# Performance work log

Measured on AMD Instinct MI355X. Metric: run time of the kernel, lower is better.

Reference implementation:

```python
import jax, jax.numpy as jnp
import numpy as np

N, IN, HID, OUT, HD = 512, 256, 256, 256, 64  # n_agents, in_dim, hid_dim, out_dim, head_dim (out_dim // n_heads)


def _mlp2(x, w1, b1, w2, b2):
    return jax.nn.relu(x @ w1.T + b1) @ w2.T + b2


def setup_inputs():
    key = jax.random.key(0)
    ks = jax.random.split(key, 32)
    p = lambda i, shape: jax.random.normal(ks[i], shape, dtype=jnp.float32) * 0.05
    V = jax.random.normal(ks[0], (N, IN), dtype=jnp.float32)
    adj = jax.random.randint(ks[1], (N, N), 0, 2, dtype=jnp.int32)
    adj = adj.at[jnp.arange(N), jnp.arange(N)].set(1)  # self-loops so no softmax row is all -inf
    prev_hidden = jax.random.normal(ks[2], (N, HID), dtype=jnp.float32)
    return {
        "V": V, "adj": adj, "prev_hidden": prev_hidden,
        "W1": p(3, (HID, IN)), "sa0": p(4, (HID,)), "sa1": p(5, (HID,)),
        "ce_w1": p(6, (HID, 2 * IN)), "ce_b1": p(7, (HID,)), "ce_w2": p(8, (HD, HID)), "ce_b2": p(9, (HD,)),
        "ca0": p(10, (HD,)), "ca1": p(11, (HD,)),
        "te_w1": p(12, (HID, IN + HID)), "te_b1": p(13, (HID,)), "te_w2": p(14, (HD, HID)), "te_b2": p(15, (HD,)),
        "ta0": p(16, (HD,)), "ta1": p(17, (HD,)),
        "pe_w1": p(18, (HID, 3 * IN)), "pe_b1": p(19, (HID,)), "pe_w2": p(20, (HD, HID)), "pe_b2": p(21, (HD,)),
        "pa0": p(22, (HD,)), "pa1": p(23, (HD,)),
        "W2": p(24, (OUT, HID + 2 * HD + 1)), "op_w": p(25, (OUT, OUT)), "op_b": p(26, (OUT,)),
        "ln_g": jnp.ones((OUT,), jnp.float32), "ln_b": jnp.zeros((OUT,), jnp.float32),
    }


def _forward(V, adj, prev_hidden, W1, sa0, sa1, ce_w1, ce_b1, ce_w2, ce_b2, ca0, ca1,
             te_w1, te_b1, te_w2, te_b2, ta0, ta1, pe_w1, pe_b1, pe_w2, pe_b2, pa0, pa1,
             W2, op_w, op_b, ln_g, ln_b):
    neg = -jnp.inf
    # --- branch 1: standard GAT attention ---
    Wh1 = V @ W1.T                                             # (N, HID)
    s1 = (Wh1 @ sa0)[:, None] + (Wh1 @ sa1)[None, :]           # (N, N)
    s1 = jnp.where(adj == 0, neg, s1)
    H1 = jax.nn.softmax(s1, axis=1) @ Wh1                      # (N, HID)
    # --- branch 2: causal, all ordered pairs i != j ---
    wA, wB = ce_w1[:, :IN], ce_w1[:, IN:]
    h = jax.nn.relu((V @ wA.T)[:, None, :] + (V @ wB.T)[None, :, :] + ce_b1)  # (N, N, HID)
    f = h @ ce_w2.T + ce_b2                                    # (N, N, HD)
    s2 = jnp.where(jnp.eye(N, dtype=bool), neg, f @ (ca0 + ca1))
    a2 = jax.nn.softmax(s2.reshape(-1)).reshape(N, N)          # softmax over all off-diagonal pairs
    H2 = jnp.broadcast_to(jnp.einsum('ij,ijd->d', a2, f), (N, HD))
    # --- branch 3: temporal; (N,1) scores broadcast against (N,N) causal mask ---
    tf = _mlp2(jnp.concatenate([V, prev_hidden], -1), te_w1, te_b1, te_w2, te_b2)  # (N, HD)
    ts = tf @ (ta0 + ta1)                                      # (N,)
    cmask = jnp.triu(jnp.ones((N, N), dtype=bool), 1)
    s3 = jnp.where(cmask, neg, jnp.broadcast_to(ts[:, None], (N, N)))
    H3 = jax.nn.softmax(s3, axis=1) @ tf                       # (N, HD) == prefix means of tf
    # --- branch 4: cooperative; first two neighbors in index order (zeros if < 2) ---
    pos = jnp.where(adj == 1, jnp.arange(N)[None, :], N)
    srt = jnp.sort(pos, axis=1)
    i0, i1 = srt[:, 0], srt[:, 1]
    valid = (i1 < N)[:, None]
    n0 = jnp.where(valid, V[jnp.clip(i0, 0, N - 1)], 0.0)
    n1 = jnp.where(valid, V[jnp.clip(i1, 0, N - 1)], 0.0)
    cf = _mlp2(jnp.concatenate([V, n0, n1], -1), pe_w1, pe_b1, pe_w2, pe_b2)  # (N, HD)
    # torch: softmax over dim of size 1 -> all ones, alpha^T @ cf == column sums -> (HD,)
    # then unsqueezed to (HD,1) and zero-padded to (N,1) since HD < N  (faithful to source bug)
    H4v = cf.sum(axis=0)
    H4 = jnp.concatenate([H4v, jnp.zeros((N - HD,), V.dtype)])[:, None]       # (N, 1)
    # --- combine ---
    Hc = jnp.concatenate([H1, H2, H3, H4], axis=-1) @ W2.T     # (N, OUT)
    out = Hc @ op_w.T + op_b
    mu = out.mean(-1, keepdims=True)
    var = ((out - mu) ** 2).mean(-1, keepdims=True)
    y = (out - mu) / jnp.sqrt(var + 1e-5) * ln_g + ln_b        # LayerNorm, eps=1e-5
    return jax.nn.elu(y)                                       # dropout is identity in eval


def reference(V, adj, prev_hidden, W1, sa0, sa1, ce_w1, ce_b1, ce_w2, ce_b2, ca0, ca1,
              te_w1, te_b1, te_w2, te_b2, ta0, ta1, pe_w1, pe_b1, pe_w2, pe_b2, pa0, pa1,
              W2, op_w, op_b, ln_g, ln_b):
    return _forward(V, adj, prev_hidden, W1, sa0, sa1, ce_w1, ce_b1, ce_w2, ce_b2, ca0, ca1,
                    te_w1, te_b1, te_w2, te_b2, ta0, ta1, pe_w1, pe_b1, pe_w2, pe_b2, pa0, pa1,
                    W2, op_w, op_b, ln_g, ln_b)
```

## Files before the change

kernel.cpp:

```cpp
#include <hip/hip_runtime.h>

typedef unsigned short u16;

constexpr int kN   = 512;
constexpr int kIN  = 256;
constexpr int kHID = 256;
constexpr int kHD  = 64;
constexpr int kOUT = 256;

__device__ __forceinline__ float us2f(u16 u){
  union { unsigned int i; float f; } c; c.i = ((unsigned int)u) << 16; return c.f;
}
__device__ __forceinline__ u16 f2us(float f){
  union { float f; unsigned int i; } c; c.f = f;
  unsigned int r = c.i + 0x7fff + ((c.i >> 16) & 1);
  return (u16)(r >> 16);
}

__device__ bool probe_is_f32(const unsigned int* __restrict__ V){
  __shared__ int cnt;
  if (threadIdx.x == 0) cnt = 0;
  __syncthreads();
  int c = 0;
  for (int k = threadIdx.x; k < 4096; k += 256){
    float x = us2f((u16)(V[k] & 0xffffu));
    if (!(fabsf(x) <= 32.0f)) c++;
  }
  atomicAdd(&cnt, c);
  __syncthreads();
  return cnt > 64;
}

struct ConvArgs { const void* src[23]; float* dst[23]; int n[23]; };

__global__ __launch_bounds__(256) void k_conv(ConvArgs a, const unsigned int* __restrict__ Vraw,
                                              const int* __restrict__ adj, int* __restrict__ flag,
                                              float* __restrict__ Xp)
{
  int b = blockIdx.x, tid = threadIdx.x;
  bool f32 = probe_is_f32(Vraw);
  if (b < 256){
    if (b == 0 && tid == 0) *flag = f32 ? 1 : 0;
    int t = b*256 + tid;
    const int stride = 65536;
    for (int s = 0; s < 23; ++s){
      int n4 = a.n[s] >> 2;
      float4* d = (float4*)a.dst[s];
      if (f32){
        const float4* sf = (const float4*)a.src[s];
        for (int i = t; i < n4; i += stride) d[i] = sf[i];
      } else {
        const ushort4* sb = (const ushort4*)a.src[s];
        for (int i = t; i < n4; i += stride){
          ushort4 u = sb[i];
          d[i] = make_float4(us2f(u.x), us2f(u.y), us2f(u.z), us2f(u.w));
        }
      }
    }
  } else {
    __shared__ unsigned long long msk[8];
    __shared__ int sj[2];
    int i = b - 256;
    int w = tid >> 6, lane = tid & 63;
    unsigned long long m0 = __ballot(adj[(size_t)i*kN + tid] != 0);
    unsigned long long m1 = __ballot(adj[(size_t)i*kN + 256 + tid] != 0);
    if (lane == 0){ msk[w] = m0; msk[4 + w] = m1; }
    __syncthreads();
    if (tid == 0){
      int j0 = -1, j1 = -1;
      for (int c = 0; c < 8 && j1 < 0; ++c){
        unsigned long long m = msk[c];
        while (m && j1 < 0){
          int bb = __builtin_ctzll(m);
          int j = c*64 + bb;
          if (j0 < 0) j0 = j; else j1 = j;
          m &= m - 1;
        }
      }
      if (j1 < 0) j0 = -1;
      sj[0] = j0; sj[1] = j1;
    }
    __syncthreads();
    int j0 = sj[0], j1 = sj[1];
    const float* Vf = (const float*)Vraw;
    const u16*  Vb = (const u16*)Vraw;
    auto rdV = [&](int r, int k)->float{
      return f32 ? Vf[(size_t)r*kIN + k] : us2f(Vb[(size_t)r*kIN + k]);
    };
    Xp[(size_t)i*768 + tid]       = rdV(i, tid);
    Xp[(size_t)i*768 + 256 + tid] = (j0 >= 0) ? rdV(j0, tid) : 0.f;
    Xp[(size_t)i*768 + 512 + tid] = (j1 >= 0) ? rdV(j1, tid) : 0.f;
  }
}

__device__ __forceinline__ float blk_red(float v, float* tmp, bool isMax){
  int lane = threadIdx.x & 63, wv = threadIdx.x >> 6;
  #pragma unroll
  for (int o = 32; o > 0; o >>= 1){
    float t = __shfl_down(v, o, 64);
    v = isMax ? fmaxf(v, t) : (v + t);
  }
  __syncthreads();
  if (lane == 0) tmp[wv] = v;
  __syncthreads();
  float r = tmp[0];
  for (int i = 1; i < 4; ++i) r = isMax ? fmaxf(r, tmp[i]) : (r + tmp[i]);
  return r;
}

struct WSP {
  const int* adj; const int* flag; void* out;
  float *Vf,*prevf,*W1f,*sa1f,*cw1f,*cb1f,*cw2f,*cb2f,*ca0f,*ca1f;
  float *tw1f,*tb1f,*tw2f,*tb2f,*pw1f,*pb1f,*pw2f,*pb2f;
  float *W2f,*opwf,*opbf,*lngf,*lnbf;
  float *tw2t,*pw2t,*W2t;
  float *Wh1,*e1v,*minv,*invzv,*H1p,*H1,*Am,*Bm,*uvec,*beta;
  float *s2,*maxp,*zp,*MZ,*gsum;
  float *htp0,*htp1,*hpp0,*hpp1,*hpp2,*hidden_t,*hidden_p;
  float *tfm,*cfm,*H3,*H4v,*Xp;
};

struct GSeg2 { const float* X; const float* W; float* C; int ldx, ldw, ldc, K; };
struct GArgs2 { GSeg2 s[8]; };

__global__ __launch_bounds__(256) void k_gemmA(GArgs2 ga)
{
  __shared__ __align__(16) float Xs[2][32][36];
  __shared__ __align__(16) float Ws[2][32][68];
  const GSeg2 sg = ga.s[blockIdx.y];
  const int tm = blockIdx.x & 15;
  const int tn = blockIdx.x >> 4;
  const int i0 = tm << 5;
  const int n0 = tn << 6;
  const int tid = threadIdx.x;

  const int xrow = tid >> 3;
  const int xk   = (tid & 7) << 2;
  const int rg = (tid >> 4) << 1;
  const int cg = (tid & 15) << 2;

  const float* Xb = sg.X + (size_t)i0 * sg.ldx;
  const float* Wb = sg.W + (size_t)n0 * sg.ldw;

  float4 xr, wr0, wr1;
  auto loadT = [&](int kt){
    xr  = *(const float4*)(Xb + (size_t)xrow * sg.ldx + kt + xk);
    wr0 = *(const float4*)(Wb + (size_t)xrow * sg.ldw + kt + xk);
    wr1 = *(const float4*)(Wb + (size_t)(xrow+32) * sg.ldw + kt + xk);
  };
  auto writeT = [&](int bu){
    Xs[bu][xk+0][xrow] = xr.x;  Xs[bu][xk+1][xrow] = xr.y;
    Xs[bu][xk+2][xrow] = xr.z;  Xs[bu][xk+3][xrow] = xr.w;
    Ws[bu][xk+0][xrow]    = wr0.x; Ws[bu][xk+1][xrow]    = wr0.y;
    Ws[bu][xk+2][xrow]    = wr0.z; Ws[bu][xk+3][xrow]    = wr0.w;
    Ws[bu][xk+0][xrow+32] = wr1.x; Ws[bu][xk+1][xrow+32] = wr1.y;
    Ws[bu][xk+2][xrow+32] = wr1.z; Ws[bu][xk+3][xrow+32] = wr1.w;
  };

  loadT(0); writeT(0); __syncthreads();

  float acc[2][4] = {};
  const int nkt = sg.K >> 5;
  for (int t = 0; t < nkt; ++t){
    if (t + 1 < nkt) loadT((t + 1) << 5);
    const int bu = t & 1;
    #pragma unroll
    for (int kk = 0; kk < 32; ++kk){
      const float2 av = *(const float2*)&Xs[bu][kk][rg];
      const float4 bv = *(const float4*)&Ws[bu][kk][cg];
      acc[0][0]+=av.x*bv.x; acc[0][1]+=av.x*bv.y; acc[0][2]+=av.x*bv.z; acc[0][3]+=av.x*bv.w;
      acc[1][0]+=av.y*bv.x; acc[1][1]+=av.y*bv.y; acc[1][2]+=av.y*bv.z; acc[1][3]+=av.y*bv.w;
    }
    if (t + 1 < nkt) writeT((t + 1) & 1);
    __syncthreads();
  }

  #pragma unroll
  for (int ri = 0; ri < 2; ++ri)
    *(float4*)(sg.C + (size_t)(i0 + rg + ri) * sg.ldc + (n0 + cg)) =
      make_float4(acc[ri][0], acc[ri][1], acc[ri][2], acc[ri][3]);
}

__global__ __launch_bounds__(256) void k_stage2(WSP w)
{
  __shared__ float st[64*65];
  int b = blockIdx.x, tid = threadIdx.x;
  if (b < 128){
    int f = b*256 + tid;
    int c4 = f & 63;
    {
      float4 a = ((const float4*)w.htp0)[f], bb = ((const float4*)w.htp1)[f];
      float4 bi = ((const float4*)w.tb1f)[c4];
      ((float4*)w.hidden_t)[f] = make_float4(
        fmaxf(a.x+bb.x+bi.x,0.f), fmaxf(a.y+bb.y+bi.y,0.f),
        fmaxf(a.z+bb.z+bi.z,0.f), fmaxf(a.w+bb.w+bi.w,0.f));
    }
    {
      float4 a = ((const float4*)w.hpp0)[f], bb = ((const float4*)w.hpp1)[f];
      float4 c = ((const float4*)w.hpp2)[f];
      float4 bi = ((const float4*)w.pb1f)[c4];
      ((float4*)w.hidden_p)[f] = make_float4(
        fmaxf(a.x+bb.x+c.x+bi.x,0.f), fmaxf(a.y+bb.y+c.y+bi.y,0.f),
        fmaxf(a.z+bb.z+c.z+bi.z,0.f), fmaxf(a.w+bb.w+c.w+bi.w,0.f));
    }
  } else if (b < 256){
    int r = (b-128)*4 + (tid >> 6), lane = tid & 63;
    float a = 0.f;
    for (int k = lane; k < kHID; k += 64) a += w.Wh1[(size_t)r*kHID + k] * w.sa1f[k];
    #pragma unroll
    for (int o = 32; o > 0; o >>= 1) a += __shfl_down(a, o, 64);
    if (lane == 0) w.e1v[r] = a;
  } else if (b == 256){
    if (tid < 64){ st[tid] = w.ca0f[tid] + w.ca1f[tid]; w.H4v[tid] = 0.f; }
    __syncthreads();
    float a = 0.f;
    for (int d = 0; d < kHD; ++d) a += w.cw2f[(size_t)d*kHID + tid] * st[d];
    w.uvec[tid] = a;
    if (tid == 0){
      float bsum = 0.f;
      for (int d = 0; d < kHD; ++d) bsum += w.cb2f[d] * st[d];
      *w.beta = bsum;
    }
  } else if (b < 259){
    const float* src = (b == 257) ? w.tw2f : w.pw2f;
    float* dst = (b == 257) ? w.tw2t : w.pw2t;
    for (int ch = 0; ch < 4; ++ch){
      __syncthreads();
      #pragma unroll
      for (int e = 0; e < 16; ++e){
        int lin = e*256 + tid;
        int r = lin >> 6, c = lin & 63;
        st[r*65 + c] = src[(size_t)r*256 + ch*64 + c];
      }
      __syncthreads();
      #pragma unroll
      for (int e = 0; e < 16; ++e){
        int lin = e*256 + tid;
        int kc = lin >> 6, dd = lin & 63;
        dst[(size_t)(ch*64 + kc)*64 + dd] = st[dd*65 + kc];
      }
    }
  } else {
    int c0 = (b - 259) * 4;
    for (int cc = 0; cc < 4; ++cc){
      int c = c0 + cc;
      if (c < 385) w.W2t[(size_t)c*256 + tid] = w.W2f[(size_t)tid*385 + c];
    }
  }
}

__global__ __launch_bounds__(256) void k_stage3(WSP w)
{
  __shared__ __align__(16) float smem3[4*256 + 256];
  int b = blockIdx.x, tid = threadIdx.x;
  if (b < 64){
    int m = b >> 5, grp = b & 31;
    const float* X  = m ? w.hidden_p : w.hidden_t;
    const float* Wt = m ? w.pw2t : w.tw2t;
    const float* bi = m ? w.pb2f : w.tb2f;
    float* C = m ? w.cfm : w.tfm;
    int i0 = grp*16 + (tid >> 6)*4;
    int d = tid & 63;
    const float* x0 = X + (size_t)i0*256;
    const float* x1 = x0 + 256;
    const float* x2 = x0 + 512;
    const float* x3 = x0 + 768;
    float a0=0.f, a1=0.f, a2=0.f, a3=0.f;
    for (int k = 0; k < 256; k += 4){
      float w0 = Wt[(size_t)(k+0)*64 + d];
      float w1 = Wt[(size_t)(k+1)*64 + d];
      float w2 = Wt[(size_t)(k+2)*64 + d];
      float w3 = Wt[(size_t)(k+3)*64 + d];
      float4 f0 = *(const float4*)(x0 + k);
      float4 f1 = *(const float4*)(x1 + k);
      float4 f2 = *(const float4*)(x2 + k);
      float4 f3 = *(const float4*)(x3 + k);
      a0 += f0.x*w0 + f0.y*w1 + f0.z*w2 + f0.w*w3;
      a1 += f1.x*w0 + f1.y*w1 + f1.z*w2 + f1.w*w3;
      a2 += f2.x*w0 + f2.y*w1 + f2.z*w2 + f2.w*w3;
      a3 += f3.x*w0 + f3.y*w1 + f3.z*w2 + f3.w*w3;
    }
    float bd = bi[d];
    C[(size_t)(i0+0)*64 + d] = a0 + bd;
    C[(size_t)(i0+1)*64 + d] = a1 + bd;
    C[(size_t)(i0+2)*64 + d] = a2 + bd;
    C[(size_t)(i0+3)*64 + d] = a3 + bd;
  } else if (b < 576){
    float* red = smem3;
    int i = b - 64;
    int m0 = w.adj[(size_t)i*kN + tid];
    int m1 = w.adj[(size_t)i*kN + tid + 256];
    float ea = w.e1v[tid], eb = w.e1v[tid+256];
    float v0 = m0 ? ea : -1e30f;
    float v1 = m1 ? eb : -1e30f;
    float m = blk_red(fmaxf(v0, v1), red, true);
    float z = blk_red((m0 ? expf(ea-m) : 0.f) + (m1 ? expf(eb-m) : 0.f), red, false);
    if (tid == 0){ w.minv[i] = m; w.invzv[i] = 1.0f / z; }
  } else {
    float* aib = smem3;
    float* uu  = smem3 + 1024;
    int q = b - 576;
    int i0 = (q & 127) * 4, j0 = (q >> 7) * 64;
    int wv = tid >> 6, lane = tid & 63;
    uu[tid] = w.uvec[tid];
    float b1v = w.cb1f[tid];
    #pragma unroll
    for (int r = 0; r < 4; ++r) aib[r*256 + tid] = w.Am[(size_t)(i0+r)*kHID + tid] + b1v;
    __syncthreads();
    int i = i0 + wv, j = j0 + lane;
    const float4* bp = (const float4*)(w.Bm + (size_t)j*kHID);
    float acc = *w.beta;
    #pragma unroll 8
    for (int k4 = 0; k4 < kHID/4; ++k4){
      float4 bv = bp[k4];
      float4 a4 = *(const float4*)&aib[wv*256 + k4*4];
      float4 u4 = *(const float4*)&uu[k4*4];
      acc += fmaxf(a4.x+bv.x,0.f)*u4.x + fmaxf(a4.y+bv.y,0.f)*u4.y
           + fmaxf(a4.z+bv.z,0.f)*u4.z + fmaxf(a4.w+bv.w,0.f)*u4.w;
    }
    if (j == i) acc = -1e30f;
    w.s2[(size_t)i*kN + j] = acc;
    float m = acc;
    #pragma unroll
    for (int o = 32; o > 0; o >>= 1) m = fmaxf(m, __shfl_down(m, o, 64));
    m = __shfl(m, 0, 64);
    float e = expf(acc - m);
    #pragma unroll
    for (int o = 32; o > 0; o >>= 1) e += __shfl_down(e, o, 64);
    if (lane == 0){
      int pb = q*4 + wv;
      w.maxp[pb] = m; w.zp[pb] = e;
    }
  }
}

__global__ __launch_bounds__(256) void k_stage4(WSP w)
{
  __shared__ __align__(16) float smem[272];
  int b = blockIdx.x, tid = threadIdx.x;
  if (b < 8){
    int d = tid & 63, sub = tid >> 6;
    int r0 = b*64 + sub*16;
    float s = 0.f;
    #pragma unroll
    for (int e = 0; e < 16; ++e) s += w.cfm[(size_t)(r0+e)*kHD + d];
    smem[sub*64 + d] = s;
    __syncthreads();
    if (tid < 64)
      atomicAdd(&w.H4v[tid], smem[tid] + smem[64+tid] + smem[128+tid] + smem[192+tid]);
  } else if (b < 1032){
    float* wt = smem;
    int q = b - 8;
    int i0 = (q & 127) * 4, jt = q >> 7, j0 = jt * 64;
    {
      int r = tid >> 6, jj = tid & 63;
      int j = j0 + jj;
      wt[r*64 + jj] = w.adj[(size_t)(i0+r)*kN + j]
                    ? expf(w.e1v[j] - w.minv[i0+r]) * w.invzv[i0+r] : 0.f;
    }
    __syncthreads();
    float a0=0,a1=0,a2=0,a3=0;
    #pragma unroll 4
    for (int jj = 0; jj < 64; ++jj){
      float wh = w.Wh1[(size_t)(j0+jj)*kHID + tid];
      a0 += wt[jj]*wh; a1 += wt[64+jj]*wh; a2 += wt[128+jj]*wh; a3 += wt[192+jj]*wh;
    }
    size_t base = ((size_t)jt*kN + i0)*kHID + tid;
    w.H1p[base]          = a0;
    w.H1p[base + kHID]   = a1;
    w.H1p[base + 2*kHID] = a2;
    w.H1p[base + 3*kHID] = a3;
  } else {
    float* red = smem;
    float m = -1e30f;
    #pragma unroll
    for (int r = 0; r < 16; ++r) m = fmaxf(m, w.maxp[tid + 256*r]);
    m = blk_red(m, red, true);
    float z = 0.f;
    #pragma unroll
    for (int r = 0; r < 16; ++r) z += w.zp[tid + 256*r] * expf(w.maxp[tid + 256*r] - m);
    z = blk_red(z, red, false);
    if (tid == 0){ w.MZ[0] = m; w.MZ[1] = z; }
    w.gsum[tid] = 0.f;
  }
}

__global__ __launch_bounds__(256) void k_stage5(WSP w)
{
  __shared__ __align__(16) char smem[1536];
  int b = blockIdx.x, tid = threadIdx.x;
  if (b < 1024){
    float* wt = (float*)smem;
    int i0 = (b & 31) * 16, j0 = (b >> 5) * 16;
    float M = w.MZ[0], invZ = 1.0f / w.MZ[1];
    {
      int r = tid >> 4, c = tid & 15;
      wt[r*16 + c] = expf(w.s2[(size_t)(i0+r)*kN + (j0+c)] - M) * invZ;
    }
    float b1v = w.cb1f[tid];
    float aib[16];
    #pragma unroll
    for (int r = 0; r < 16; ++r) aib[r] = w.Am[(size_t)(i0+r)*kHID + tid] + b1v;
    __syncthreads();
    float acc = 0.f;
    for (int j = 0; j < 16; ++j){
      float bj = w.Bm[(size_t)(j0+j)*kHID + tid];
      #pragma unroll
      for (int r = 0; r < 16; ++r)
        acc += wt[r*16 + j] * fmaxf(aib[r] + bj, 0.f);
    }
    atomicAdd(&w.gsum[tid], acc);
  } else if (b < 1536){
    int i = b - 1024;
    float s = 0.f;
    #pragma unroll
    for (int jt = 0; jt < 8; ++jt)
      s += w.H1p[((size_t)jt*kN + i)*kHID + tid];
    w.H1[(size_t)i*kHID + tid] = s;
  } else {
    int d = b - 1536;
    int lane = tid & 63, wv = tid >> 6;
    float v0 = w.tfm[(size_t)(2*tid)*kHD + d];
    float v1 = w.tfm[(size_t)(2*tid+1)*kHD + d];
    float s = v0 + v1;
    float x = s;
    #pragma unroll
    for (int off = 1; off < 64; off <<= 1){
      float y = __shfl_up(x, off, 64);
      if (lane >= off) x += y;
    }
    float* wsum = (float*)smem;
    if (lane == 63) wsum[wv] = x;
    __syncthreads();
    float base = 0.f;
    for (int k = 0; k < wv; ++k) base += wsum[k];
    float excl = base + x - s;
    w.H3[(size_t)(2*tid)*kHD + d]   = (excl + v0) / (float)(2*tid + 1);
    w.H3[(size_t)(2*tid+1)*kHD + d] = (excl + s)  / (float)(2*tid + 2);
  }
}

__global__ __launch_bounds__(256) void k_outfin(WSP w)
{
  __shared__ float h1s[kHID];
  __shared__ float gssh[kHID];
  __shared__ float part[kHD][4];
  __shared__ float h2s[kHD];
  __shared__ float h3s[kHD];
  __shared__ float row[kOUT];
  __shared__ float red[4];
  __shared__ float h4sh;
  int i = blockIdx.x, o = threadIdx.x;
  h1s[o] = w.H1[(size_t)i*kHID + o];
  gssh[o] = w.gsum[o];
  if (o < kHD) h3s[o] = w.H3[(size_t)i*kHD + o];
  if (o == 0)  h4sh = (i < kHD) ? w.H4v[i] : 0.f;
  __syncthreads();
  {
    int dd = o >> 2, q = o & 3;
    float a = 0.f;
    for (int kk = 0; kk < 64; ++kk){
      int k = q*64 + kk;
      a += gssh[k] * w.cw2f[(size_t)dd*kHID + k];
    }
    part[dd][q] = a;
  }
  __syncthreads();
  if (o < kHD)
    h2s[o] = w.cb2f[o] + part[o][0] + part[o][1] + part[o][2] + part[o][3];
  __syncthreads();
  float acc = 0.f;
  for (int k = 0; k < kHID; ++k) acc += h1s[k] * w.W2t[(size_t)k*256 + o];
  for (int dd = 0; dd < kHD; ++dd){
    acc += h2s[dd] * w.W2t[(size_t)(256+dd)*256 + o];
    acc += h3s[dd] * w.W2t[(size_t)(320+dd)*256 + o];
  }
  acc += h4sh * w.W2t[(size_t)384*256 + o];
  row[o] = acc;
  __syncthreads();
  const float4* opr = (const float4*)(w.opwf + (size_t)o * kOUT);
  float a2 = w.opbf[o];
  for (int kb = 0; kb < 64; ++kb){
    float4 qv = opr[kb];
    a2 += row[kb*4]*qv.x + row[kb*4+1]*qv.y + row[kb*4+2]*qv.z + row[kb*4+3]*qv.w;
  }
  float mu = blk_red(a2, red, false) * (1.0f/kOUT);
  float dv = a2 - mu;
  float var = blk_red(dv*dv, red, false) * (1.0f/kOUT);
  float y = dv * rsqrtf(var + 1e-5f) * w.lngf[o] + w.lnbf[o];
  y = (y > 0.f) ? y : expm1f(y);
  if (*w.flag) ((float*)w.out)[(size_t)i*kOUT + o] = y;
  else         ((u16*)w.out)[(size_t)i*kOUT + o]   = f2us(y);
}

extern "C" void kernel_launch(void* const* d_in, const int* in_sizes, int n_in,
                              void* d_out, int out_size, void* d_ws, size_t ws_size,
                              hipStream_t stream)
{
  const void* V     = d_in[0];
  const int*  adj   = (const int*)d_in[1];
  const void* prev  = d_in[2];
  const void* W1    = d_in[3];
  const void* sa1   = d_in[5];
  const void* ce_w1 = d_in[6];
  const void* ce_b1 = d_in[7];
  const void* ce_w2 = d_in[8];
  const void* ce_b2 = d_in[9];
  const void* ca0   = d_in[10];
  const void* ca1   = d_in[11];
  const void* te_w1 = d_in[12];
  const void* te_b1 = d_in[13];
  const void* te_w2 = d_in[14];
  const void* te_b2 = d_in[15];
  const void* pe_w1 = d_in[18];
  const void* pe_b1 = d_in[19];
  const void* pe_w2 = d_in[20];
  const void* pe_b2 = d_in[21];
  const void* W2    = d_in[24];
  const void* op_w  = d_in[25];
  const void* op_b  = d_in[26];
  const void* ln_g  = d_in[27];
  const void* ln_b  = d_in[28];

  float* ws  = (float*)d_ws;
  int*  flag = (int*)ws;
  float* p   = ws + 16;
  float* Vf   = p; p += 131072;
  float* prevf= p; p += 131072;
  float* W1f  = p; p += 65536;
  float* sa1f = p; p += 256;
  float* cw1f = p; p += 131072;
  float* cb1f = p; p += 256;
  float* cw2f = p; p += 16384;
  float* cb2f = p; p += 64;
  float* ca0f = p; p += 64;
  float* ca1f = p; p += 64;
  float* tw1f = p; p += 131072;
  float* tb1f = p; p += 256;
  float* tw2f = p; p += 16384;
  float* tb2f = p; p += 64;
  float* pw1f = p; p += 196608;
  float* pb1f = p; p += 256;
  float* pw2f = p; p += 16384;
  float* pb2f = p; p += 64;
  float* W2f  = p; p += 98560;
  float* opwf = p; p += 65536;
  float* opbf = p; p += 256;
  float* lngf = p; p += 256;
  float* lnbf = p; p += 256;
  float* tw2t = p; p += 16384;
  float* pw2t = p; p += 16384;
  float* W2t  = p; p += 98560;
  float* Wh1      = p; p += 131072;
  float* e1v      = p; p += 512;
  float* minv     = p; p += 512;
  float* invzv    = p; p += 512;
  float* H1p      = p; p += 1048576;
  float* H1       = p; p += 131072;
  float* Am       = p; p += 131072;
  float* Bm       = p; p += 131072;
  float* uvec     = p; p += 256;
  float* beta     = p; p += 16;
  float* s2       = p; p += 262144;
  float* maxp     = p; p += 4096;
  float* zpart    = p; p += 4096;
  float* MZ       = p; p += 16;
  float* gsum     = p; p += 256;
  float* htp0     = p; p += 131072;
  float* htp1     = p; p += 131072;
  float* hpp0     = p; p += 131072;
  float* hpp1     = p; p += 131072;
  float* hpp2     = p; p += 131072;
  float* hidden_t = p; p += 131072;
  float* hidden_p = p; p += 131072;
  float* tfm      = p; p += 32768;
  float* cfm      = p; p += 32768;
  float* H3       = p; p += 32768;
  float* H4v      = p; p += 64;
  float* Xp       = p; p += 393216;

  WSP w;
  w.adj = adj; w.flag = flag; w.out = d_out;
  w.Vf=Vf; w.prevf=prevf; w.W1f=W1f; w.sa1f=sa1f; w.cw1f=cw1f; w.cb1f=cb1f;
  w.cw2f=cw2f; w.cb2f=cb2f; w.ca0f=ca0f; w.ca1f=ca1f;
  w.tw1f=tw1f; w.tb1f=tb1f; w.tw2f=tw2f; w.tb2f=tb2f;
  w.pw1f=pw1f; w.pb1f=pb1f; w.pw2f=pw2f; w.pb2f=pb2f;
  w.W2f=W2f; w.opwf=opwf; w.opbf=opbf; w.lngf=lngf; w.lnbf=lnbf;
  w.tw2t=tw2t; w.pw2t=pw2t; w.W2t=W2t;
  w.Wh1=Wh1; w.e1v=e1v; w.minv=minv; w.invzv=invzv; w.H1p=H1p; w.H1=H1;
  w.Am=Am; w.Bm=Bm; w.uvec=uvec; w.beta=beta;
  w.s2=s2; w.maxp=maxp; w.zp=zpart; w.MZ=MZ; w.gsum=gsum;
  w.htp0=htp0; w.htp1=htp1; w.hpp0=hpp0; w.hpp1=hpp1; w.hpp2=hpp2;
  w.hidden_t=hidden_t; w.hidden_p=hidden_p;
  w.tfm=tfm; w.cfm=cfm; w.H3=H3; w.H4v=H4v; w.Xp=Xp;

  {
    ConvArgs ca;
    const void* srcs[23] = {V, prev, W1, sa1, ce_w1, ce_b1, ce_w2, ce_b2, ca0, ca1,
                            te_w1, te_b1, te_w2, te_b2, pe_w1, pe_b1, pe_w2, pe_b2,
                            W2, op_w, op_b, ln_g, ln_b};
    float* dsts[23] = {Vf, prevf, W1f, sa1f, cw1f, cb1f, cw2f, cb2f, ca0f, ca1f,
                       tw1f, tb1f, tw2f, tb2f, pw1f, pb1f, pw2f, pb2f,
                       W2f, opwf, opbf, lngf, lnbf};
    int ns[23] = {131072, 131072, 65536, 256, 131072, 256, 16384, 64, 64, 64,
                  131072, 256, 16384, 64, 196608, 256, 16384, 64,
                  98560, 65536, 256, 256, 256};
    for (int s = 0; s < 23; ++s){ ca.src[s] = srcs[s]; ca.dst[s] = dsts[s]; ca.n[s] = ns[s]; }
    k_conv<<<768, 256, 0, stream>>>(ca, (const unsigned int*)V, adj, flag, Xp);
  }

  {
    GArgs2 g{};
    g.s[0] = {Vf,       W1f,        Wh1,  256, 256, 256, 256};
    g.s[1] = {Vf,       cw1f,       Am,   256, 512, 256, 256};
    g.s[2] = {Vf,       cw1f + 256, Bm,   256, 512, 256, 256};
    g.s[3] = {Vf,       tw1f,       htp0, 256, 512, 256, 256};
    g.s[4] = {prevf,    tw1f + 256, htp1, 256, 512, 256, 256};
    g.s[5] = {Xp,       pw1f,       hpp0, 768, 768, 256, 256};
    g.s[6] = {Xp + 256, pw1f + 256, hpp1, 768, 768, 256, 256};
    g.s[7] = {Xp + 512, pw1f + 512, hpp2, 768, 768, 256, 256};
    k_gemmA<<<dim3(64, 8), 256, 0, stream>>>(g);
  }

  k_stage2<<<356, 256, 0, stream>>>(w);

  k_stage3<<<1600, 256, 0, stream>>>(w);

  k_stage4<<<1033, 256, 0, stream>>>(w);

  k_stage5<<<1600, 256, 0, stream>>>(w);

  k_outfin<<<kN, 256, 0, stream>>>(w);
}
```

Baseline: 271.7 us.

## Replace per-row output kernel with tiled GEMMs and enlarge gemmA tile

The old k_outfin kernel, one block per row, did the W2 and op_w matvecs with poor weight reuse. It is replaced by a tiled 32x32 GEMM over a packed [H1|H3] buffer against compacted W2 columns. The H2 contribution (constant across rows) and the H4 column are folded into the op_w GEMM's input load, and a separate warp-level LayerNorm+ELU kernel finishes the output. The first-stage GEMM tile also grows from 32x64 to 64x64 per block to raise arithmetic intensity, at the cost of fewer blocks and two extra launches.

Result: faster. 244.7 us (-9.9%).

```diff
diff --git a/kernel.cpp b/kernel.cpp
--- a/kernel.cpp
+++ b/kernel.cpp
@@ -113,11 +113,11 @@
   float *Vf,*prevf,*W1f,*sa1f,*cw1f,*cb1f,*cw2f,*cb2f,*ca0f,*ca1f;
   float *tw1f,*tb1f,*tw2f,*tb2f,*pw1f,*pb1f,*pw2f,*pb2f;
   float *W2f,*opwf,*opbf,*lngf,*lnbf;
-  float *tw2t,*pw2t,*W2t;
-  float *Wh1,*e1v,*minv,*invzv,*H1p,*H1,*Am,*Bm,*uvec,*beta;
+  float *tw2t,*pw2t,*W2c,*W2midt,*w384v,*c2v;
+  float *Wh1,*e1v,*minv,*invzv,*H1p,*Hc,*Am,*Bm,*uvec,*beta;
   float *s2,*maxp,*zp,*MZ,*gsum;
   float *htp0,*htp1,*hpp0,*hpp1,*hpp2,*hidden_t,*hidden_p;
-  float *tfm,*cfm,*H3,*H4v,*Xp;
+  float *tfm,*cfm,*H4v,*Xp,*out2,*out3;
 };
 
 struct GSeg2 { const float* X; const float* W; float* C; int ldx, ldw, ldc, K; };
@@ -125,32 +125,35 @@
 
 __global__ __launch_bounds__(256) void k_gemmA(GArgs2 ga)
 {
-  __shared__ __align__(16) float Xs[2][32][36];
+  __shared__ __align__(16) float Xs[2][32][68];
   __shared__ __align__(16) float Ws[2][32][68];
   const GSeg2 sg = ga.s[blockIdx.y];
-  const int tm = blockIdx.x & 15;
-  const int tn = blockIdx.x >> 4;
-  const int i0 = tm << 5;
+  const int tm = blockIdx.x & 7;
+  const int tn = blockIdx.x >> 3;
+  const int i0 = tm << 6;
   const int n0 = tn << 6;
   const int tid = threadIdx.x;
 
   const int xrow = tid >> 3;
   const int xk   = (tid & 7) << 2;
-  const int rg = (tid >> 4) << 1;
+  const int rg = (tid >> 4) << 2;
   const int cg = (tid & 15) << 2;
 
   const float* Xb = sg.X + (size_t)i0 * sg.ldx;
   const float* Wb = sg.W + (size_t)n0 * sg.ldw;
 
-  float4 xr, wr0, wr1;
+  float4 xr0, xr1, wr0, wr1;
   auto loadT = [&](int kt){
-    xr  = *(const float4*)(Xb + (size_t)xrow * sg.ldx + kt + xk);
+    xr0 = *(const float4*)(Xb + (size_t)xrow * sg.ldx + kt + xk);
+    xr1 = *(const float4*)(Xb + (size_t)(xrow+32) * sg.ldx + kt + xk);
     wr0 = *(const float4*)(Wb + (size_t)xrow * sg.ldw + kt + xk);
     wr1 = *(const float4*)(Wb + (size_t)(xrow+32) * sg.ldw + kt + xk);
   };
   auto writeT = [&](int bu){
-    Xs[bu][xk+0][xrow] = xr.x;  Xs[bu][xk+1][xrow] = xr.y;
-    Xs[bu][xk+2][xrow] = xr.z;  Xs[bu][xk+3][xrow] = xr.w;
+    Xs[bu][xk+0][xrow] = xr0.x;  Xs[bu][xk+1][xrow] = xr0.y;
+    Xs[bu][xk+2][xrow] = xr0.z;  Xs[bu][xk+3][xrow] = xr0.w;
+    Xs[bu][xk+0][xrow+32] = xr1.x;  Xs[bu][xk+1][xrow+32] = xr1.y;
+    Xs[bu][xk+2][xrow+32] = xr1.z;  Xs[bu][xk+3][xrow+32] = xr1.w;
     Ws[bu][xk+0][xrow]    = wr0.x; Ws[bu][xk+1][xrow]    = wr0.y;
     Ws[bu][xk+2][xrow]    = wr0.z; Ws[bu][xk+3][xrow]    = wr0.w;
     Ws[bu][xk+0][xrow+32] = wr1.x; Ws[bu][xk+1][xrow+32] = wr1.y;
@@ -159,26 +162,84 @@
 
   loadT(0); writeT(0); __syncthreads();
 
-  float acc[2][4] = {};
+  float acc[4][4] = {};
   const int nkt = sg.K >> 5;
   for (int t = 0; t < nkt; ++t){
     if (t + 1 < nkt) loadT((t + 1) << 5);
     const int bu = t & 1;
     #pragma unroll
     for (int kk = 0; kk < 32; ++kk){
-      const float2 av = *(const float2*)&Xs[bu][kk][rg];
+      const float4 av = *(const float4*)&Xs[bu][kk][rg];
       const float4 bv = *(const float4*)&Ws[bu][kk][cg];
       acc[0][0]+=av.x*bv.x; acc[0][1]+=av.x*bv.y; acc[0][2]+=av.x*bv.z; acc[0][3]+=av.x*bv.w;
       acc[1][0]+=av.y*bv.x; acc[1][1]+=av.y*bv.y; acc[1][2]+=av.y*bv.z; acc[1][3]+=av.y*bv.w;
+      acc[2][0]+=av.z*bv.x; acc[2][1]+=av.z*bv.y; acc[2][2]+=av.z*bv.z; acc[2][3]+=av.z*bv.w;
+      acc[3][0]+=av.w*bv.x; acc[3][1]+=av.w*bv.y; acc[3][2]+=av.w*bv.z; acc[3][3]+=av.w*bv.w;
     }
     if (t + 1 < nkt) writeT((t + 1) & 1);
     __syncthreads();
   }
 
   #pragma unroll
-  for (int ri = 0; ri < 2; ++ri)
+  for (int ri = 0; ri < 4; ++ri)
     *(float4*)(sg.C + (size_t)(i0 + rg + ri) * sg.ldc + (n0 + cg)) =
       make_float4(acc[ri][0], acc[ri][1], acc[ri][2], acc[ri][3]);
+}
+
+struct GS32 { const float* X; const float* W; float* C; int ldx, ldw, ldc, K;
+              const float* c2; const float* w384; const float* h4; };
+
+__device__ __forceinline__ void gemm32_body(const GS32 sg, int tm, int tn, int tid,
+                                            float* Xs, float* Ws)
+{
+  const int i0 = tm << 5, n0 = tn << 5;
+  const int xrow = tid >> 3;
+  const int xk = (tid & 7) << 2;
+  const int rg = (tid >> 4) << 1;
+  const int cg = (tid & 15) << 1;
+  const float* Xb = sg.X + (size_t)i0 * sg.ldx;
+  const float* Wb = sg.W + (size_t)n0 * sg.ldw;
+  float h4r = 0.f;
+  if (sg.h4){ int i = i0 + xrow; h4r = (i < 64) ? sg.h4[i] : 0.f; }
+  float4 xr, wr;
+  auto loadT = [&](int kt){
+    xr = *(const float4*)(Xb + (size_t)xrow * sg.ldx + kt + xk);
+    wr = *(const float4*)(Wb + (size_t)xrow * sg.ldw + kt + xk);
+    if (sg.c2){
+      float4 c = *(const float4*)(sg.c2 + kt + xk);
+      float4 w3 = *(const float4*)(sg.w384 + kt + xk);
+      xr.x += c.x + h4r*w3.x; xr.y += c.y + h4r*w3.y;
+      xr.z += c.z + h4r*w3.z; xr.w += c.w + h4r*w3.w;
+    }
+  };
+  auto writeT = [&](int bu){
+    float* xs = Xs + bu*1152;
+    xs[(xk+0)*36 + xrow] = xr.x; xs[(xk+1)*36 + xrow] = xr.y;
+    xs[(xk+2)*36 + xrow] = xr.z; xs[(xk+3)*36 + xrow] = xr.w;
+    float* wsp = Ws + bu*1152;
+    wsp[(xk+0)*36 + xrow] = wr.x; wsp[(xk+1)*36 + xrow] = wr.y;
+    wsp[(xk+2)*36 + xrow] = wr.z; wsp[(xk+3)*36 + xrow] = wr.w;
+  };
+  loadT(0); writeT(0); __syncthreads();
+  float a00=0,a01=0,a10=0,a11=0;
+  const int nkt = sg.K >> 5;
+  for (int t = 0; t < nkt; ++t){
+    if (t+1 < nkt) loadT((t+1) << 5);
+    const float* xs = Xs + (t&1)*1152;
+    const float* wsp = Ws + (t&1)*1152;
+    #pragma unroll
+    for (int kk = 0; kk < 32; ++kk){
+      float2 av = *(const float2*)&xs[kk*36 + rg];
+      float2 bv = *(const float2*)&wsp[kk*36 + cg];
+      a00 += av.x*bv.x; a01 += av.x*bv.y;
+      a10 += av.y*bv.x; a11 += av.y*bv.y;
+    }
+    if (t+1 < nkt) writeT((t+1)&1);
+    __syncthreads();
+  }
+  float* cp = sg.C + (size_t)(i0+rg)*sg.ldc + n0 + cg;
+  *(float2*)cp = make_float2(a00, a01);
+  *(float2*)(cp + sg.ldc) = make_float2(a10, a11);
 }
 
 __global__ __launch_bounds__(256) void k_stage2(WSP w)
@@ -240,12 +301,22 @@
         dst[(size_t)(ch*64 + kc)*64 + dd] = st[dd*65 + kc];
       }
     }
+  } else if (b < 323){
+    int o0 = (b - 259) * 4;
+    for (int r = 0; r < 4; ++r){
+      int o = o0 + r;
+      const float* src = w.W2f + (size_t)o * 385;
+      float* dst = w.W2c + (size_t)o * 320;
+      for (int c = tid; c < 320; c += 256)
+        dst[c] = src[(c < 256) ? c : c + 64];
+    }
+  } else if (b < 339){
+    int d0 = (b - 323) * 4;
+    #pragma unroll
+    for (int dd = 0; dd < 4; ++dd)
+      w.W2midt[(size_t)(d0+dd)*256 + tid] = w.W2f[(size_t)tid*385 + 256 + d0 + dd];
   } else {
-    int c0 = (b - 259) * 4;
-    for (int cc = 0; cc < 4; ++cc){
-      int c = c0 + cc;
-      if (c < 385) w.W2t[(size_t)c*256 + tid] = w.W2f[(size_t)tid*385 + c];
-    }
+    w.w384v[tid] = w.W2f[(size_t)tid*385 + 384];
   }
 }
 
@@ -416,7 +487,7 @@
     #pragma unroll
     for (int jt = 0; jt < 8; ++jt)
       s += w.H1p[((size_t)jt*kN + i)*kHID + tid];
-    w.H1[(size_t)i*kHID + tid] = s;
+    w.Hc[(size_t)i*320 + tid] = s;
   } else {
     int d = b - 1536;
     int lane = tid & 63, wv = tid >> 6;
@@ -435,62 +506,78 @@
     float base = 0.f;
     for (int k = 0; k < wv; ++k) base += wsum[k];
     float excl = base + x - s;
-    w.H3[(size_t)(2*tid)*kHD + d]   = (excl + v0) / (float)(2*tid + 1);
-    w.H3[(size_t)(2*tid+1)*kHD + d] = (excl + s)  / (float)(2*tid + 2);
-  }
-}
-
-__global__ __launch_bounds__(256) void k_outfin(WSP w)
-{
-  __shared__ float h1s[kHID];
-  __shared__ float gssh[kHID];
-  __shared__ float part[kHD][4];
-  __shared__ float h2s[kHD];
-  __shared__ float h3s[kHD];
-  __shared__ float row[kOUT];
-  __shared__ float red[4];
-  __shared__ float h4sh;
-  int i = blockIdx.x, o = threadIdx.x;
-  h1s[o] = w.H1[(size_t)i*kHID + o];
-  gssh[o] = w.gsum[o];
-  if (o < kHD) h3s[o] = w.H3[(size_t)i*kHD + o];
-  if (o == 0)  h4sh = (i < kHD) ? w.H4v[i] : 0.f;
-  __syncthreads();
-  {
-    int dd = o >> 2, q = o & 3;
+    w.Hc[(size_t)(2*tid)*320 + 256 + d]   = (excl + v0) / (float)(2*tid + 1);
+    w.Hc[(size_t)(2*tid+1)*320 + 256 + d] = (excl + s)  / (float)(2*tid + 2);
+  }
+}
+
+__global__ __launch_bounds__(256) void k_out2g(WSP w)
+{
+  __shared__ __align__(16) char smem[18432];
+  int b = blockIdx.x, tid = threadIdx.x;
+  if (b < 128){
+    GS32 sg{w.Hc, w.W2c, w.out2, 320, 320, 256, 320, nullptr, nullptr, nullptr};
+    gemm32_body(sg, b & 15, b >> 4, tid, (float*)smem, (float*)(smem + 9216));
+  } else {
+    float* gs  = (float*)smem;
+    float* part= (float*)(smem + 1024);
+    float* h2s = (float*)(smem + 2048);
+    gs[tid] = w.gsum[tid];
+    __syncthreads();
+    int dd = tid >> 2, q = tid & 3;
     float a = 0.f;
     for (int kk = 0; kk < 64; ++kk){
       int k = q*64 + kk;
-      a += gssh[k] * w.cw2f[(size_t)dd*kHID + k];
-    }
-    part[dd][q] = a;
-  }
-  __syncthreads();
-  if (o < kHD)
-    h2s[o] = w.cb2f[o] + part[o][0] + part[o][1] + part[o][2] + part[o][3];
-  __syncthreads();
-  float acc = 0.f;
-  for (int k = 0; k < kHID; ++k) acc += h1s[k] * w.W2t[(size_t)k*256 + o];
-  for (int dd = 0; dd < kHD; ++dd){
-    acc += h2s[dd] * w.W2t[(size_t)(256+dd)*256 + o];
-    acc += h3s[dd] * w.W2t[(size_t)(320+dd)*256 + o];
-  }
-  acc += h4sh * w.W2t[(size_t)384*256 + o];
-  row[o] = acc;
-  __syncthreads();
-  const float4* opr = (const float4*)(w.opwf + (size_t)o * kOUT);
-  float a2 = w.opbf[o];
-  for (int kb = 0; kb < 64; ++kb){
-    float4 qv = opr[kb];
-    a2 += row[kb*4]*qv.x + row[kb*4+1]*qv.y + row[kb*4+2]*qv.z + row[kb*4+3]*qv.w;
-  }
-  float mu = blk_red(a2, red, false) * (1.0f/kOUT);
-  float dv = a2 - mu;
-  float var = blk_red(dv*dv, red, false) * (1.0f/kOUT);
-  float y = dv * rsqrtf(var + 1e-5f) * w.lngf[o] + w.lnbf[o];
-  y = (y > 0.f) ? y : expm1f(y);
-  if (*w.flag) ((float*)w.out)[(size_t)i*kOUT + o] = y;
-  else         ((u16*)w.out)[(size_t)i*kOUT + o]   = f2us(y);
+      a += gs[k] * w.cw2f[(size_t)dd*kHID + k];
+    }
+    part[dd*4 + q] = a;
+    __syncthreads();
+    if (tid < kHD)
+      h2s[tid] = w.cb2f[tid] + part[tid*4] + part[tid*4+1] + part[tid*4+2] + part[tid*4+3];
+    __syncthreads();
+    float c = 0.f;
+    for (int d = 0; d < kHD; ++d) c += h2s[d] * w.W2midt[(size_t)d*256 + tid];
+    w.c2v[tid] = c;
+  }
+}
+
+__global__ __launch_bounds__(256) void k_out3g(WSP w)
+{
+  __shared__ __align__(16) char smem[18432];
+  GS32 sg{w.out2, w.opwf, w.out3, 256, 256, 256, 256, w.c2v, w.w384v, w.H4v};
+  gemm32_body(sg, blockIdx.x & 15, blockIdx.x >> 4, threadIdx.x, (float*)smem, (float*)(smem + 9216));
+}
+
+__global__ __launch_bounds__(256) void k_final(WSP w)
+{
+  int b = blockIdx.x, tid = threadIdx.x;
+  int row = b*4 + (tid >> 6), lane = tid & 63;
+  float4 v = *(const float4*)(w.out3 + (size_t)row*kOUT + lane*4);
+  float4 pb = *(const float4*)(w.opbf + lane*4);
+  v.x += pb.x; v.y += pb.y; v.z += pb.z; v.w += pb.w;
+  float s = v.x + v.y + v.z + v.w;
+  #pragma unroll
+  for (int o = 32; o > 0; o >>= 1) s += __shfl_xor(s, o, 64);
+  float mu = s * (1.0f/kOUT);
+  float dx = v.x-mu, dy = v.y-mu, dz = v.z-mu, dw = v.w-mu;
+  float ss = dx*dx + dy*dy + dz*dz + dw*dw;
+  #pragma unroll
+  for (int o = 32; o > 0; o >>= 1) ss += __shfl_xor(ss, o, 64);
+  float rs = rsqrtf(ss * (1.0f/kOUT) + 1e-5f);
+  float4 g = *(const float4*)(w.lngf + lane*4);
+  float4 be = *(const float4*)(w.lnbf + lane*4);
+  float y0 = dx*rs*g.x + be.x, y1 = dy*rs*g.y + be.y;
+  float y2 = dz*rs*g.z + be.z, y3 = dw*rs*g.w + be.w;
+  y0 = (y0 > 0.f) ? y0 : expm1f(y0);
+  y1 = (y1 > 0.f) ? y1 : expm1f(y1);
+  y2 = (y2 > 0.f) ? y2 : expm1f(y2);
+  y3 = (y3 > 0.f) ? y3 : expm1f(y3);
+  if (*w.flag){
+    *(float4*)((float*)w.out + (size_t)row*kOUT + lane*4) = make_float4(y0,y1,y2,y3);
+  } else {
+    ushort4 u; u.x = f2us(y0); u.y = f2us(y1); u.z = f2us(y2); u.w = f2us(y3);
+    ((ushort4*)w.out)[(size_t)row*64 + lane] = u;
+  }
 }
 
 extern "C" void kernel_launch(void* const* d_in, const int* in_sizes, int n_in,
@@ -550,13 +637,16 @@
   float* lnbf = p; p += 256;
   float* tw2t = p; p += 16384;
   float* pw2t = p; p += 16384;
-  float* W2t  = p; p += 98560;
+  float* W2c  = p; p += 81920;
+  float* W2midt = p; p += 16384;
+  float* w384v  = p; p += 256;
+  float* c2v    = p; p += 256;
   float* Wh1      = p; p += 131072;
   float* e1v      = p; p += 512;
   float* minv     = p; p += 512;
   float* invzv    = p; p += 512;
   float* H1p      = p; p += 1048576;
-  float* H1       = p; p += 131072;
+  float* Hc       = p; p += 163840;
   float* Am       = p; p += 131072;
   float* Bm       = p; p += 131072;
   float* uvec     = p; p += 256;
@@ -575,9 +665,10 @@
   float* hidden_p = p; p += 131072;
   float* tfm      = p; p += 32768;
   float* cfm      = p; p += 32768;
-  float* H3       = p; p += 32768;
   float* H4v      = p; p += 64;
   float* Xp       = p; p += 393216;
+  float* out2     = p; p += 131072;
+  float* out3     = p; p += 131072;
 
   WSP w;
   w.adj = adj; w.flag = flag; w.out = d_out;
@@ -586,13 +677,13 @@
   w.tw1f=tw1f; w.tb1f=tb1f; w.tw2f=tw2f; w.tb2f=tb2f;
   w.pw1f=pw1f; w.pb1f=pb1f; w.pw2f=pw2f; w.pb2f=pb2f;
   w.W2f=W2f; w.opwf=opwf; w.opbf=opbf; w.lngf=lngf; w.lnbf=lnbf;
-  w.tw2t=tw2t; w.pw2t=pw2t; w.W2t=W2t;
-  w.Wh1=Wh1; w.e1v=e1v; w.minv=minv; w.invzv=invzv; w.H1p=H1p; w.H1=H1;
+  w.tw2t=tw2t; w.pw2t=pw2t; w.W2c=W2c; w.W2midt=W2midt; w.w384v=w384v; w.c2v=c2v;
+  w.Wh1=Wh1; w.e1v=e1v; w.minv=minv; w.invzv=invzv; w.H1p=H1p; w.Hc=Hc;
   w.Am=Am; w.Bm=Bm; w.uvec=uvec; w.beta=beta;
   w.s2=s2; w.maxp=maxp; w.zp=zpart; w.MZ=MZ; w.gsum=gsum;
   w.htp0=htp0; w.htp1=htp1; w.hpp0=hpp0; w.hpp1=hpp1; w.hpp2=hpp2;
   w.hidden_t=hidden_t; w.hidden_p=hidden_p;
-  w.tfm=tfm; w.cfm=cfm; w.H3=H3; w.H4v=H4v; w.Xp=Xp;
+  w.tfm=tfm; w.cfm=cfm; w.H4v=H4v; w.Xp=Xp; w.out2=out2; w.out3=out3;
 
   {
     ConvArgs ca;
@@ -619,10 +710,10 @@
     g.s[5] = {Xp,       pw1f,       hpp0, 768, 768, 256, 256};
     g.s[6] = {Xp + 256, pw1f + 256, hpp1, 768, 768, 256, 256};
     g.s[7] = {Xp + 512, pw1f + 512, hpp2, 768, 768, 256, 256};
-    k_gemmA<<<dim3(64, 8), 256, 0, stream>>>(g);
-  }
-
-  k_stage2<<<356, 256, 0, stream>>>(w);
+    k_gemmA<<<dim3(32, 8), 256, 0, stream>>>(g);
+  }
+
+  k_stage2<<<340, 256, 0, stream>>>(w);
 
   k_stage3<<<1600, 256, 0, stream>>>(w);
 
@@ -630,5 +721,9 @@
 
   k_stage5<<<1600, 256, 0, stream>>>(w);
 
-  k_outfin<<<kN, 256, 0, stream>>>(w);
-}
+  k_out2g<<<129, 256, 0, stream>>>(w);
+
+  k_out3g<<<128, 256, 0, stream>>>(w);
+
+  k_final<<<128, 256, 0, stream>>>(w);
+}
```
